# Kernel optimization log

Hardware: AMD Instinct MI355X
Metric: run time of the kernel (lower is better)

## Reference

```python
import jax, jax.numpy as jnp
import numpy as np

B, T, D, V, L = 32, 512, 512, 1024, 128
BLANK = 0
NEG = -1e30  # log-domain 'minus infinity' that is fp-safe


def setup_inputs() -> dict:
    key = jax.random.key(0)
    k1, k2, k3 = jax.random.split(key, 3)
    x = jax.random.normal(k1, (B, T, D), dtype=jnp.float32)
    W = jax.random.normal(k2, (D, V), dtype=jnp.float32) / np.sqrt(D).astype(np.float32)
    b = jnp.zeros((V,), dtype=jnp.float32)
    # CTC targets must be in [1, V) (never the blank id 0)
    target = jax.random.randint(k3, (B, L), 1, V)
    input_lengths = jnp.full((B,), T, dtype=jnp.int32)
    target_lengths = jnp.full((B,), L, dtype=jnp.int32)
    return {"x": x, "W": W, "b": b, "target": target,
            "input_lengths": input_lengths, "target_lengths": target_lengths}


def _ctc_loss(log_probs, target, input_lengths, target_lengths):
    # log_probs: [T, B, V] (time-major), target: [B, L]
    Tt, Bb, _ = log_probs.shape
    Ll = target.shape[1]
    S = 2 * Ll + 1  # extended label sequence: blank,t0,blank,t1,...,blank
    ext = jnp.full((Bb, S), BLANK, dtype=target.dtype).at[:, 1::2].set(target)  # [B,S]
    ext_m2 = jnp.pad(ext, ((0, 0), (2, 0)), constant_values=BLANK)[:, :S]
    skip = (ext != BLANK) & (ext != ext_m2) & (jnp.arange(S)[None, :] >= 2)  # [B,S]

    # gather log-probs of extended labels for every time step: [T,B,S]
    lp_ext = jnp.take_along_axis(log_probs, jnp.broadcast_to(ext[None], (Tt, Bb, S)), axis=2)

    alpha0 = jnp.full((Bb, S), NEG, log_probs.dtype)
    alpha0 = alpha0.at[:, 0].set(lp_ext[0, :, 0]).at[:, 1].set(lp_ext[0, :, 1])

    def step(alpha, lp_t):
        a1 = jnp.pad(alpha, ((0, 0), (1, 0)), constant_values=NEG)[:, :S]
        a2 = jnp.pad(alpha, ((0, 0), (2, 0)), constant_values=NEG)[:, :S]
        c = jnp.logaddexp(alpha, a1)
        c = jnp.where(skip, jnp.logaddexp(c, a2), c)
        new = c + lp_t
        return new, new

    _, alphas = jax.lax.scan(step, alpha0, lp_ext[1:])
    alphas = jnp.concatenate([alpha0[None], alphas], axis=0)  # [T,B,S]

    bi = jnp.arange(Bb)
    a_last = alphas[input_lengths - 1, bi]  # [B,S] alpha at each sample's final frame
    ll = jnp.logaddexp(a_last[bi, 2 * target_lengths - 1], a_last[bi, 2 * target_lengths])
    nll = -ll  # per-sample negative log-likelihood
    # zero_infinity=True: infinite losses are zeroed
    nll = jnp.where(jnp.isinf(nll) | (nll > 1e29), 0.0, nll)
    # reduction='mean': divide each loss by its target length, then mean
    return jnp.mean(nll / jnp.maximum(target_lengths, 1).astype(nll.dtype))


def reference(x, W, b, target, input_lengths, target_lengths):
    logits = jnp.einsum('btd,dv->btv', x, W) + b  # nn.Linear
    log_probs = jax.nn.log_softmax(logits, axis=-1)  # [B,T,V]
    return _ctc_loss(jnp.transpose(log_probs, (1, 0, 2)), target, input_lengths, target_lengths)
```

## Files before the change

kernel.cpp:

```cpp
#include <hip/hip_runtime.h>
#include <cstdint>


#define SPAD 260
#define PEXT_PAD_ROWS 64
#define L2E 1.4426950408889634f
#define LN2 0.6931471805599453f

typedef short v8s __attribute__((ext_vector_type(8)));
typedef float v4f __attribute__((ext_vector_type(4)));

__device__ __forceinline__ uint32_t f2bf_bits(float f) {
  uint32_t u = __float_as_uint(f);
  return (u + 0x7FFFu + ((u >> 16) & 1u)) >> 16;
}
__device__ __forceinline__ float bf2f(uint32_t h) { return __uint_as_float(h << 16); }

__global__ void k_prep(const float* __restrict__ x, uint16_t* __restrict__ xb, long long n,
                       const float* __restrict__ W, uint16_t* __restrict__ Wt, int D, int V,
                       float* __restrict__ out, int nconv) {
  if (blockIdx.x == 0 && threadIdx.x == 0) out[0] = 0.f;
  if ((int)blockIdx.x < nconv) {
    long long i = ((long long)blockIdx.x * blockDim.x + threadIdx.x) * 8;
    if (i >= n) return;
    float4 a = *(const float4*)(x + i);
    float4 b = *(const float4*)(x + i + 4);
    uint4 o;
    o.x = f2bf_bits(a.x) | (f2bf_bits(a.y) << 16);
    o.y = f2bf_bits(a.z) | (f2bf_bits(a.w) << 16);
    o.z = f2bf_bits(b.x) | (f2bf_bits(b.y) << 16);
    o.w = f2bf_bits(b.z) | (f2bf_bits(b.w) << 16);
    *(uint4*)(xb + i) = o;
  } else {
    __shared__ float tile[32][33];
    const int bid2 = blockIdx.x - nconv;
    const int n0 = (bid2 % (V / 32)) * 32, k0 = (bid2 / (V / 32)) * 32;
    const int tx = threadIdx.x & 31, ty = threadIdx.x >> 5;
    #pragma unroll
    for (int i = 0; i < 32; i += 8)
      tile[ty + i][tx] = W[(size_t)(k0 + ty + i) * V + n0 + tx];
    __syncthreads();
    #pragma unroll
    for (int i = 0; i < 32; i += 8)
      Wt[(size_t)(n0 + ty + i) * D + k0 + tx] = (uint16_t)f2bf_bits(tile[tx][ty + i]);
  }
}

__global__ __launch_bounds__(256) void k_gemm(const uint16_t* __restrict__ A,
                                              const uint16_t* __restrict__ Bt,
                                              const float* __restrict__ bias,
                                              uint16_t* __restrict__ C, int M, int N, int K) {
  __shared__ uint16_t As[128 * 32];
  __shared__ uint16_t Bs[128 * 32];
  const int tid = threadIdx.x, lane = tid & 63, wave = tid >> 6;
  const int m0 = blockIdx.x * 128, n0 = blockIdx.y * 128;
  const int wm = wave & 1, wn = wave >> 1;
  const int frow = lane & 15, kb = lane >> 4;
  const int lr = lane >> 2, kc = lane & 3;
  v4f acc[4][4] = {};

  for (int k0 = 0; k0 < K; k0 += 32) {
    __syncthreads();
    #pragma unroll
    for (int i = 0; i < 2; i++) {
      const int r = (wave * 2 + i) * 16 + lr;
      const uint16_t* ga = A + (size_t)(m0 + r) * K + k0 + kc * 8;
      const uint16_t* gb = Bt + (size_t)(n0 + r) * K + k0 + kc * 8;
      __builtin_amdgcn_global_load_lds(
          (const __attribute__((address_space(1))) void*)ga,
          (__attribute__((address_space(3))) void*)(As + (wave * 2 + i) * 512 + lane * 8), 16, 0, 0);
      __builtin_amdgcn_global_load_lds(
          (const __attribute__((address_space(1))) void*)gb,
          (__attribute__((address_space(3))) void*)(Bs + (wave * 2 + i) * 512 + lane * 8), 16, 0, 0);
    }
    __syncthreads();

    v8s af[4], bf[4];
    #pragma unroll
    for (int i = 0; i < 4; i++)
      af[i] = *(const v8s*)(As + (wm * 64 + i * 16 + frow) * 32 + kb * 8);
    #pragma unroll
    for (int j = 0; j < 4; j++)
      bf[j] = *(const v8s*)(Bs + (wn * 64 + j * 16 + frow) * 32 + kb * 8);
    #pragma unroll
    for (int i = 0; i < 4; i++)
      #pragma unroll
      for (int j = 0; j < 4; j++)
        acc[i][j] = __builtin_amdgcn_mfma_f32_16x16x32_bf16(af[i], bf[j], acc[i][j], 0, 0, 0);
  }

  const int crow = (lane >> 4) * 4, ccol = lane & 15;
  #pragma unroll
  for (int j = 0; j < 4; j++) {
    const int n = n0 + wn * 64 + j * 16 + ccol;
    const float bv = bias[n];
    #pragma unroll
    for (int i = 0; i < 4; i++) {
      const int mb = m0 + wm * 64 + i * 16 + crow;
      #pragma unroll
      for (int r2 = 0; r2 < 4; r2++)
        C[(size_t)(mb + r2) * N + n] = (uint16_t)f2bf_bits(acc[i][j][r2] + bv);
    }
  }
}

__global__ void k_softmax_gather(const uint16_t* __restrict__ logits, const int* __restrict__ target,
                                 const int* __restrict__ tlen, float* __restrict__ pext,
                                 int T, int V, int L) {
  const int row = blockIdx.x * 4 + (threadIdx.x >> 6);
  const int lane = threadIdx.x & 63;
  const uint16_t* lrow = logits + (size_t)row * V;

  float xs[16];
  int cnt = 0;
  float mx = -INFINITY;
  for (int base = 0; base < V; base += 256) {
    const int idx = base + lane * 4;
    uint2 u = *(const uint2*)(lrow + idx);
    float4 v;
    v.x = bf2f(u.x & 0xFFFFu); v.y = bf2f(u.x >> 16);
    v.z = bf2f(u.y & 0xFFFFu); v.w = bf2f(u.y >> 16);
    xs[cnt] = v.x; xs[cnt + 1] = v.y; xs[cnt + 2] = v.z; xs[cnt + 3] = v.w; cnt += 4;
    mx = fmaxf(mx, fmaxf(fmaxf(v.x, v.y), fmaxf(v.z, v.w)));
  }
  #pragma unroll
  for (int off = 32; off; off >>= 1) mx = fmaxf(mx, __shfl_xor(mx, off, 64));
  float sum = 0.f;
  #pragma unroll
  for (int q = 0; q < 16; q++) { if (q < cnt) sum += exp2f((xs[q] - mx) * L2E); }
  #pragma unroll
  for (int off = 32; off; off >>= 1) sum += __shfl_xor(sum, off, 64);
  const float lse2 = mx * L2E + log2f(sum);

  const int bidx = row / T;
  const int Lb = tlen[bidx];
  const int S = 2 * Lb + 1;
  float* prow = pext + (size_t)row * SPAD;
  for (int s = lane; s < SPAD; s += 64) {
    float p = 0.f;
    if (s < S) {
      const int lbl = (s & 1) ? target[bidx * L + ((s - 1) >> 1)] : 0;
      p = exp2f(bf2f(lrow[lbl]) * L2E - lse2);
    }
    prow[s] = p;
  }
}

__device__ __forceinline__ float wave_shr1(float x) {
  return __int_as_float(__builtin_amdgcn_update_dpp(0, __float_as_int(x), 0x138, 0xf, 0xf, true));
}
__device__ __forceinline__ float wave_max_nonneg(float x) {
  x = fmaxf(x, __int_as_float(__builtin_amdgcn_update_dpp(0, __float_as_int(x), 0x111, 0xf, 0xf, true)));
  x = fmaxf(x, __int_as_float(__builtin_amdgcn_update_dpp(0, __float_as_int(x), 0x112, 0xf, 0xf, true)));
  x = fmaxf(x, __int_as_float(__builtin_amdgcn_update_dpp(0, __float_as_int(x), 0x114, 0xf, 0xf, true)));
  x = fmaxf(x, __int_as_float(__builtin_amdgcn_update_dpp(0, __float_as_int(x), 0x118, 0xf, 0xf, true)));
  x = fmaxf(x, __int_as_float(__builtin_amdgcn_update_dpp(0, __float_as_int(x), 0x142, 0xf, 0xf, true)));
  x = fmaxf(x, __int_as_float(__builtin_amdgcn_update_dpp(0, __float_as_int(x), 0x143, 0xf, 0xf, true)));
  return __int_as_float(__builtin_amdgcn_readlane(__float_as_int(x), 63));
}

__device__ __forceinline__ void load8(float4* __restrict__ p, float* __restrict__ p4,
                                      const float* __restrict__ pb, int t0, int lane) {
  #pragma unroll
  for (int k = 0; k < 8; k++) {
    const float* row = pb + (size_t)(t0 + k) * SPAD;
    p[k] = *(const float4*)(row + (lane << 2));
    p4[k] = row[256];
  }
}

__global__ __launch_bounds__(64, 1) void k_ctc(const float* __restrict__ pext,
                                               const int* __restrict__ target,
                                               const int* __restrict__ ilen,
                                               const int* __restrict__ tlen,
                                               float* __restrict__ out, int T, int L) {
  const int b = blockIdx.x;
  const int lane = threadIdx.x;
  const int B = gridDim.x;
  const int Tb = ilen[b];
  const int Lb = tlen[b];
  const int S = 2 * Lb + 1;
  const int* tg = target + b * L;

  const int s1 = 4 * lane + 1, s3 = 4 * lane + 3;
  float sk1 = 0.f, sk3 = 0.f;
  if (s1 >= 3 && s1 < S) sk1 = (tg[(s1 - 1) >> 1] != tg[(s1 - 3) >> 1]) ? 1.f : 0.f;
  if (s3 >= 3 && s3 < S) sk3 = (tg[(s3 - 1) >> 1] != tg[(s3 - 3) >> 1]) ? 1.f : 0.f;

  const float* pb = pext + (size_t)b * T * SPAD;
  const float4 p0 = *(const float4*)(pb + (lane << 2));
  float a0 = (lane == 0) ? p0.x : 0.f;
  float a1 = (lane == 0) ? p0.y : 0.f;
  float a2 = 0.f, a3 = 0.f, a4 = 0.f;
  float log2C = 0.f;

  #define CTC_STEP(PP, P4) {                                            \
    const float pm3 = wave_shr1(a3);                                    \
    const float a255 = __int_as_float(__builtin_amdgcn_readlane(__float_as_int(a3), 63)); \
    const float n0v = (a0 + pm3) * (PP).x;                              \
    const float n1v = (a1 + a0 + sk1 * pm3) * (PP).y;                   \
    const float n2v = (a2 + a1) * (PP).z;                               \
    const float n3v = (a3 + a2 + sk3 * a1) * (PP).w;                    \
    const float n4v = (a4 + a255) * (P4);                               \
    a0 = n0v; a1 = n1v; a2 = n2v; a3 = n3v; a4 = n4v; }

  #define RENORM {                                                      \
    float m = fmaxf(fmaxf(fmaxf(a0, a1), fmaxf(a2, a3)), a4);           \
    m = wave_max_nonneg(m);                                             \
    const int e = (int)((__float_as_uint(m) >> 23) & 255u) - 127;       \
    const float scale = __uint_as_float((uint32_t)(127 - e) << 23);     \
    a0 *= scale; a1 *= scale; a2 *= scale; a3 *= scale; a4 *= scale;    \
    log2C += (float)e; }

  float4 Pa[8], Pb_[8], Pc[8], Pd[8];
  float Qa[8], Qb[8], Qc[8], Qd[8];
  int t0 = 1;
  bool done = false;
  load8(Pa, Qa, pb, t0, lane);
  load8(Pb_, Qb, pb, t0 + 8, lane);
  load8(Pc, Qc, pb, t0 + 16, lane);

  #define PHASE(LP, LQ, CP, CQ) {                                       \
    if (t0 + 8 <= Tb) {                                                 \
      load8(LP, LQ, pb, t0 + 24, lane);                                 \
      _Pragma("unroll")                                                 \
      for (int k = 0; k < 8; k++) CTC_STEP(CP[k], CQ[k]);               \
      RENORM; t0 += 8;                                                  \
    } else {                                                            \
      _Pragma("unroll")                                                 \
      for (int k = 0; k < 8; k++) { if (t0 + k < Tb) CTC_STEP(CP[k], CQ[k]); } \
      RENORM; done = true;                                              \
    } }

  while (!done) {
    PHASE(Pd, Qd, Pa, Qa); if (done) break;
    PHASE(Pa, Qa, Pb_, Qb); if (done) break;
    PHASE(Pb_, Qb, Pc, Qc); if (done) break;
    PHASE(Pc, Qc, Pd, Qd);
  }

  __shared__ float abuf[257];
  abuf[4 * lane + 0] = a0; abuf[4 * lane + 1] = a1;
  abuf[4 * lane + 2] = a2; abuf[4 * lane + 3] = a3;
  if (lane == 63) abuf[256] = a4;
  __syncthreads();
  if (lane == 0) {
    const float ssum = abuf[2 * Lb - 1] + abuf[2 * Lb];
    const float ll = (log2f(ssum) + log2C) * LN2;
    float nll = -ll;
    if (!(nll < 1e29f)) nll = 0.f;
    atomicAdd(out, nll / ((float)(Lb > 0 ? Lb : 1) * (float)B));
  }
}

extern "C" void kernel_launch(void* const* d_in, const int* in_sizes, int n_in,
                              void* d_out, int out_size, void* d_ws, size_t ws_size,
                              hipStream_t stream) {
  const float* x      = (const float*)d_in[0];
  const float* W      = (const float*)d_in[1];
  const float* bias   = (const float*)d_in[2];
  const int*  target  = (const int*)d_in[3];
  const int*  ilen    = (const int*)d_in[4];
  const int*  tlen    = (const int*)d_in[5];

  const int B = in_sizes[4];
  const int V = in_sizes[2];
  const int D = in_sizes[1] / V;
  const int T = in_sizes[0] / (B * D);
  const int L = in_sizes[3] / B;
  const int M = B * T;

  char* ws = (char*)d_ws;
  const size_t xb_bytes = (size_t)M * D * 2;
  const size_t wt_bytes = (size_t)V * D * 2;
  const size_t pext_bytes = (size_t)(M + PEXT_PAD_ROWS) * SPAD * 4;
  uint16_t* xb = (uint16_t*)ws;
  uint16_t* Wt = (uint16_t*)(ws + xb_bytes);
  uint16_t* logits = (uint16_t*)(ws + xb_bytes + wt_bytes);
  const size_t log_bytes = (size_t)M * V * 2;

  float* pext;
  if (pext_bytes <= xb_bytes + wt_bytes) {
    pext = (float*)ws;
  } else {
    pext = (float*)(ws + xb_bytes + wt_bytes + log_bytes);
  }

  const long long nx = (long long)M * D;
  const int nconv = (int)((nx / 8 + 255) / 256);
  const int ntrans = (V / 32) * (D / 32);
  k_prep<<<nconv + ntrans, 256, 0, stream>>>(x, xb, nx, W, Wt, D, V, (float*)d_out, nconv);
  k_gemm<<<dim3(M / 128, V / 128), 256, 0, stream>>>(xb, Wt, bias, logits, M, V, D);
  k_softmax_gather<<<M / 4, 256, 0, stream>>>(logits, target, tlen, pext, T, V, L);
  k_ctc<<<B, 64, 0, stream>>>(pext, target, ilen, tlen, (float*)d_out, T, L);
}
```

Baseline: 169.9 us.

## Fuse x conversion, GEMM, log-softmax and label gather into one kernel

Replaces the separate x-to-bf16 conversion, tiled GEMM and softmax/gather kernels with one kernel in which each block computes a full 32-row by 1024-column logits tile. The block converts x on the fly, takes the row max and sum-exp from registers, and gathers the label probabilities from an LDS tile. This removes the round trips of the bf16 x copy and the full logits matrix through global memory, plus two launches. In exchange it drops LDS staging of operands, so W fragments are read straight from global/L2 with little reuse. It also uses a large LDS tile and 128 accumulator registers per thread, which limits occupancy to about one block per CU.

```diff
diff --git a/kernel.cpp b/kernel.cpp
--- a/kernel.cpp
+++ b/kernel.cpp
@@ -4,6 +4,7 @@
 
 #define SPAD 260
 #define PEXT_PAD_ROWS 64
+#define TSTRIDE 36
 #define L2E 1.4426950408889634f
 #define LN2 0.6931471805599453f
 
@@ -16,133 +17,134 @@
 }
 __device__ __forceinline__ float bf2f(uint32_t h) { return __uint_as_float(h << 16); }
 
-__global__ void k_prep(const float* __restrict__ x, uint16_t* __restrict__ xb, long long n,
-                       const float* __restrict__ W, uint16_t* __restrict__ Wt, int D, int V,
-                       float* __restrict__ out, int nconv) {
+__device__ __forceinline__ v8s pack_bf8(float4 lo, float4 hi) {
+  union { v8s v; uint16_t s[8]; } u;
+  u.s[0] = (uint16_t)f2bf_bits(lo.x); u.s[1] = (uint16_t)f2bf_bits(lo.y);
+  u.s[2] = (uint16_t)f2bf_bits(lo.z); u.s[3] = (uint16_t)f2bf_bits(lo.w);
+  u.s[4] = (uint16_t)f2bf_bits(hi.x); u.s[5] = (uint16_t)f2bf_bits(hi.y);
+  u.s[6] = (uint16_t)f2bf_bits(hi.z); u.s[7] = (uint16_t)f2bf_bits(hi.w);
+  return u.v;
+}
+
+__global__ void k_prep(const float* __restrict__ W, uint16_t* __restrict__ Wt, int D, int V,
+                       float* __restrict__ out) {
   if (blockIdx.x == 0 && threadIdx.x == 0) out[0] = 0.f;
-  if ((int)blockIdx.x < nconv) {
-    long long i = ((long long)blockIdx.x * blockDim.x + threadIdx.x) * 8;
-    if (i >= n) return;
-    float4 a = *(const float4*)(x + i);
-    float4 b = *(const float4*)(x + i + 4);
-    uint4 o;
-    o.x = f2bf_bits(a.x) | (f2bf_bits(a.y) << 16);
-    o.y = f2bf_bits(a.z) | (f2bf_bits(a.w) << 16);
-    o.z = f2bf_bits(b.x) | (f2bf_bits(b.y) << 16);
-    o.w = f2bf_bits(b.z) | (f2bf_bits(b.w) << 16);
-    *(uint4*)(xb + i) = o;
-  } else {
-    __shared__ float tile[32][33];
-    const int bid2 = blockIdx.x - nconv;
-    const int n0 = (bid2 % (V / 32)) * 32, k0 = (bid2 / (V / 32)) * 32;
-    const int tx = threadIdx.x & 31, ty = threadIdx.x >> 5;
-    #pragma unroll
-    for (int i = 0; i < 32; i += 8)
-      tile[ty + i][tx] = W[(size_t)(k0 + ty + i) * V + n0 + tx];
-    __syncthreads();
-    #pragma unroll
-    for (int i = 0; i < 32; i += 8)
-      Wt[(size_t)(n0 + ty + i) * D + k0 + tx] = (uint16_t)f2bf_bits(tile[tx][ty + i]);
-  }
-}
-
-__global__ __launch_bounds__(256) void k_gemm(const uint16_t* __restrict__ A,
-                                              const uint16_t* __restrict__ Bt,
-                                              const float* __restrict__ bias,
-                                              uint16_t* __restrict__ C, int M, int N, int K) {
-  __shared__ uint16_t As[128 * 32];
-  __shared__ uint16_t Bs[128 * 32];
+  __shared__ float tile[32][33];
+  const int n0 = (blockIdx.x % (V / 32)) * 32, k0 = (blockIdx.x / (V / 32)) * 32;
+  const int tx = threadIdx.x & 31, ty = threadIdx.x >> 5;
+  #pragma unroll
+  for (int i = 0; i < 32; i += 8)
+    tile[ty + i][tx] = W[(size_t)(k0 + ty + i) * V + n0 + tx];
+  __syncthreads();
+  #pragma unroll
+  for (int i = 0; i < 32; i += 8)
+    Wt[(size_t)(n0 + ty + i) * D + k0 + tx] = (uint16_t)f2bf_bits(tile[tx][ty + i]);
+}
+
+__global__ __launch_bounds__(256, 1) void k_fused(const float* __restrict__ x,
+                                                  const uint16_t* __restrict__ Wt,
+                                                  const float* __restrict__ bias,
+                                                  const int* __restrict__ target,
+                                                  const int* __restrict__ tlen,
+                                                  float* __restrict__ pext,
+                                                  int T, int V, int K, int L) {
   const int tid = threadIdx.x, lane = tid & 63, wave = tid >> 6;
-  const int m0 = blockIdx.x * 128, n0 = blockIdx.y * 128;
-  const int wm = wave & 1, wn = wave >> 1;
-  const int frow = lane & 15, kb = lane >> 4;
-  const int lr = lane >> 2, kc = lane & 3;
-  v4f acc[4][4] = {};
+  const int q = lane >> 4, c = lane & 15;
+  const int m0 = blockIdx.x * 32;
+  const int nw = wave * 256;
+
+  v4f acc[2][16] = {};
+
+  const float* xa0 = x + (size_t)(m0 + c) * K + q * 8;
+  const float* xa1 = x + (size_t)(m0 + 16 + c) * K + q * 8;
 
   for (int k0 = 0; k0 < K; k0 += 32) {
-    __syncthreads();
-    #pragma unroll
-    for (int i = 0; i < 2; i++) {
-      const int r = (wave * 2 + i) * 16 + lr;
-      const uint16_t* ga = A + (size_t)(m0 + r) * K + k0 + kc * 8;
-      const uint16_t* gb = Bt + (size_t)(n0 + r) * K + k0 + kc * 8;
-      __builtin_amdgcn_global_load_lds(
-          (const __attribute__((address_space(1))) void*)ga,
-          (__attribute__((address_space(3))) void*)(As + (wave * 2 + i) * 512 + lane * 8), 16, 0, 0);
-      __builtin_amdgcn_global_load_lds(
-          (const __attribute__((address_space(1))) void*)gb,
-          (__attribute__((address_space(3))) void*)(Bs + (wave * 2 + i) * 512 + lane * 8), 16, 0, 0);
-    }
-    __syncthreads();
-
-    v8s af[4], bf[4];
-    #pragma unroll
-    for (int i = 0; i < 4; i++)
-      af[i] = *(const v8s*)(As + (wm * 64 + i * 16 + frow) * 32 + kb * 8);
-    #pragma unroll
-    for (int j = 0; j < 4; j++)
-      bf[j] = *(const v8s*)(Bs + (wn * 64 + j * 16 + frow) * 32 + kb * 8);
-    #pragma unroll
-    for (int i = 0; i < 4; i++)
-      #pragma unroll
-      for (int j = 0; j < 4; j++)
-        acc[i][j] = __builtin_amdgcn_mfma_f32_16x16x32_bf16(af[i], bf[j], acc[i][j], 0, 0, 0);
-  }
-
-  const int crow = (lane >> 4) * 4, ccol = lane & 15;
-  #pragma unroll
-  for (int j = 0; j < 4; j++) {
-    const int n = n0 + wn * 64 + j * 16 + ccol;
-    const float bv = bias[n];
-    #pragma unroll
-    for (int i = 0; i < 4; i++) {
-      const int mb = m0 + wm * 64 + i * 16 + crow;
-      #pragma unroll
-      for (int r2 = 0; r2 < 4; r2++)
-        C[(size_t)(mb + r2) * N + n] = (uint16_t)f2bf_bits(acc[i][j][r2] + bv);
-    }
-  }
-}
-
-__global__ void k_softmax_gather(const uint16_t* __restrict__ logits, const int* __restrict__ target,
-                                 const int* __restrict__ tlen, float* __restrict__ pext,
-                                 int T, int V, int L) {
-  const int row = blockIdx.x * 4 + (threadIdx.x >> 6);
-  const int lane = threadIdx.x & 63;
-  const uint16_t* lrow = logits + (size_t)row * V;
-
-  float xs[16];
-  int cnt = 0;
-  float mx = -INFINITY;
-  for (int base = 0; base < V; base += 256) {
-    const int idx = base + lane * 4;
-    uint2 u = *(const uint2*)(lrow + idx);
-    float4 v;
-    v.x = bf2f(u.x & 0xFFFFu); v.y = bf2f(u.x >> 16);
-    v.z = bf2f(u.y & 0xFFFFu); v.w = bf2f(u.y >> 16);
-    xs[cnt] = v.x; xs[cnt + 1] = v.y; xs[cnt + 2] = v.z; xs[cnt + 3] = v.w; cnt += 4;
-    mx = fmaxf(mx, fmaxf(fmaxf(v.x, v.y), fmaxf(v.z, v.w)));
-  }
-  #pragma unroll
-  for (int off = 32; off; off >>= 1) mx = fmaxf(mx, __shfl_xor(mx, off, 64));
-  float sum = 0.f;
-  #pragma unroll
-  for (int q = 0; q < 16; q++) { if (q < cnt) sum += exp2f((xs[q] - mx) * L2E); }
-  #pragma unroll
-  for (int off = 32; off; off >>= 1) sum += __shfl_xor(sum, off, 64);
-  const float lse2 = mx * L2E + log2f(sum);
-
-  const int bidx = row / T;
-  const int Lb = tlen[bidx];
+    const v8s af0 = pack_bf8(*(const float4*)(xa0 + k0), *(const float4*)(xa0 + k0 + 4));
+    const v8s af1 = pack_bf8(*(const float4*)(xa1 + k0), *(const float4*)(xa1 + k0 + 4));
+    #pragma unroll
+    for (int jj = 0; jj < 16; jj++) {
+      const v8s bf = *(const v8s*)(Wt + (size_t)(nw + jj * 16 + c) * K + k0 + q * 8);
+      acc[0][jj] = __builtin_amdgcn_mfma_f32_16x16x32_bf16(af0, bf, acc[0][jj], 0, 0, 0);
+      acc[1][jj] = __builtin_amdgcn_mfma_f32_16x16x32_bf16(af1, bf, acc[1][jj], 0, 0, 0);
+    }
+  }
+
+  float bv[16];
+  #pragma unroll
+  for (int jj = 0; jj < 16; jj++) bv[jj] = bias[nw + jj * 16 + c];
+  #pragma unroll
+  for (int i = 0; i < 2; i++)
+    #pragma unroll
+    for (int jj = 0; jj < 16; jj++)
+      #pragma unroll
+      for (int r = 0; r < 4; r++) acc[i][jj][r] += bv[jj];
+
+  float mx[2][4], sm[2][4];
+  #pragma unroll
+  for (int i = 0; i < 2; i++)
+    #pragma unroll
+    for (int r = 0; r < 4; r++) {
+      float m = -INFINITY;
+      #pragma unroll
+      for (int jj = 0; jj < 16; jj++) m = fmaxf(m, acc[i][jj][r]);
+      #pragma unroll
+      for (int off = 1; off < 16; off <<= 1) m = fmaxf(m, __shfl_xor(m, off, 64));
+      float s = 0.f;
+      #pragma unroll
+      for (int jj = 0; jj < 16; jj++) s += exp2f((acc[i][jj][r] - m) * L2E);
+      #pragma unroll
+      for (int off = 1; off < 16; off <<= 1) s += __shfl_xor(s, off, 64);
+      mx[i][r] = m; sm[i][r] = s;
+    }
+
+  __shared__ uint16_t ltile[1024 * TSTRIDE];
+  __shared__ float red_mx[4][32], red_sm[4][32], lse2s[32];
+
+  #pragma unroll
+  for (int i = 0; i < 2; i++)
+    #pragma unroll
+    for (int jj = 0; jj < 16; jj++) {
+      union { uint16_t s[4]; uint64_t u; } pk;
+      #pragma unroll
+      for (int r = 0; r < 4; r++) pk.s[r] = (uint16_t)f2bf_bits(acc[i][jj][r]);
+      *(uint64_t*)(ltile + (size_t)(nw + jj * 16 + c) * TSTRIDE + i * 16 + 4 * q) = pk.u;
+    }
+  if (c == 0) {
+    #pragma unroll
+    for (int i = 0; i < 2; i++)
+      #pragma unroll
+      for (int r = 0; r < 4; r++) {
+        red_mx[wave][16 * i + 4 * q + r] = mx[i][r];
+        red_sm[wave][16 * i + 4 * q + r] = sm[i][r];
+      }
+  }
+  __syncthreads();
+  if (tid < 32) {
+    float M = fmaxf(fmaxf(red_mx[0][tid], red_mx[1][tid]), fmaxf(red_mx[2][tid], red_mx[3][tid]));
+    float S = 0.f;
+    #pragma unroll
+    for (int w = 0; w < 4; w++) S += red_sm[w][tid] * exp2f((red_mx[w][tid] - M) * L2E);
+    lse2s[tid] = M * L2E + log2f(S);
+  }
+  __syncthreads();
+
+  const int b = m0 / T;
+  const int Lb = tlen[b];
   const int S = 2 * Lb + 1;
-  float* prow = pext + (size_t)row * SPAD;
-  for (int s = lane; s < SPAD; s += 64) {
-    float p = 0.f;
-    if (s < S) {
-      const int lbl = (s & 1) ? target[bidx * L + ((s - 1) >> 1)] : 0;
-      p = exp2f(bf2f(lrow[lbl]) * L2E - lse2);
-    }
-    prow[s] = p;
+  const int* tg = target + b * L;
+  #pragma unroll
+  for (int rr = 0; rr < 8; rr++) {
+    const int row = wave * 8 + rr;
+    const float l2 = lse2s[row];
+    float* prow = pext + (size_t)(m0 + row) * SPAD;
+    for (int s = lane; s < SPAD; s += 64) {
+      float p = 0.f;
+      if (s < S) {
+        const int lbl = (s & 1) ? tg[(s - 1) >> 1] : 0;
+        p = exp2f(bf2f(ltile[(size_t)lbl * TSTRIDE + row]) * L2E - l2);
+      }
+      prow[s] = p;
+    }
   }
 }
 
@@ -271,26 +273,11 @@
   const int M = B * T;
 
   char* ws = (char*)d_ws;
-  const size_t xb_bytes = (size_t)M * D * 2;
   const size_t wt_bytes = (size_t)V * D * 2;
-  const size_t pext_bytes = (size_t)(M + PEXT_PAD_ROWS) * SPAD * 4;
-  uint16_t* xb = (uint16_t*)ws;
-  uint16_t* Wt = (uint16_t*)(ws + xb_bytes);
-  uint16_t* logits = (uint16_t*)(ws + xb_bytes + wt_bytes);
-  const size_t log_bytes = (size_t)M * V * 2;
-
-  float* pext;
-  if (pext_bytes <= xb_bytes + wt_bytes) {
-    pext = (float*)ws;
-  } else {
-    pext = (float*)(ws + xb_bytes + wt_bytes + log_bytes);
-  }
-
-  const long long nx = (long long)M * D;
-  const int nconv = (int)((nx / 8 + 255) / 256);
-  const int ntrans = (V / 32) * (D / 32);
-  k_prep<<<nconv + ntrans, 256, 0, stream>>>(x, xb, nx, W, Wt, D, V, (float*)d_out, nconv);
-  k_gemm<<<dim3(M / 128, V / 128), 256, 0, stream>>>(xb, Wt, bias, logits, M, V, D);
-  k_softmax_gather<<<M / 4, 256, 0, stream>>>(logits, target, tlen, pext, T, V, L);
+  uint16_t* Wt = (uint16_t*)ws;
+  float* pext = (float*)(ws + wt_bytes);
+
+  k_prep<<<(V / 32) * (D / 32), 256, 0, stream>>>(W, Wt, D, V, (float*)d_out);
+  k_fused<<<M / 32, 256, 0, stream>>>(x, Wt, bias, target, tlen, pext, T, V, D, L);
   k_ctc<<<B, 64, 0, stream>>>(pext, target, ilen, tlen, (float*)d_out, T, L);
 }
```

After: 279.6 us. 1.65x slower.

## Restructure GEMM to stage full-K A tile in LDS and stream B from global

Applied to the files above, without the earlier changes.

The GEMM now uses a 64x256 block tile. The full 64xK A slab is loaded into padded LDS once, and each wave reads its B fragments straight from global memory. This removes the per-K-step double syncthreads and the shared B staging. The trade-off is a larger LDS footprint, which limits occupancy, and uncoalesced global B fragment loads. Separately, scheduling barriers are added in the CTC recurrence so the prefetch loads are issued before the compute steps.

```diff
diff --git a/kernel.cpp b/kernel.cpp
--- a/kernel.cpp
+++ b/kernel.cpp
@@ -4,6 +4,7 @@
 
 #define SPAD 260
 #define PEXT_PAD_ROWS 64
+#define ASTR 520
 #define L2E 1.4426950408889634f
 #define LN2 0.6931471805599453f
 
@@ -50,53 +51,47 @@
                                               const uint16_t* __restrict__ Bt,
                                               const float* __restrict__ bias,
                                               uint16_t* __restrict__ C, int M, int N, int K) {
-  __shared__ uint16_t As[128 * 32];
-  __shared__ uint16_t Bs[128 * 32];
+  __shared__ uint16_t As[64 * ASTR];
   const int tid = threadIdx.x, lane = tid & 63, wave = tid >> 6;
-  const int m0 = blockIdx.x * 128, n0 = blockIdx.y * 128;
-  const int wm = wave & 1, wn = wave >> 1;
+  const int m0 = blockIdx.x * 64, n0 = blockIdx.y * 256;
   const int frow = lane & 15, kb = lane >> 4;
-  const int lr = lane >> 2, kc = lane & 3;
   v4f acc[4][4] = {};
 
+  #pragma unroll
+  for (int i = 0; i < 16; i++) {
+    const int r = i * 4 + wave;
+    const uint16_t* ga = A + (size_t)(m0 + r) * K + lane * 8;
+    __builtin_amdgcn_global_load_lds(
+        (const __attribute__((address_space(1))) void*)ga,
+        (__attribute__((address_space(3))) void*)(As + r * ASTR + lane * 8), 16, 0, 0);
+  }
+  __syncthreads();
+
+  const uint16_t* Bw = Bt + (size_t)(n0 + wave * 64) * K;
+  #pragma unroll 2
   for (int k0 = 0; k0 < K; k0 += 32) {
-    __syncthreads();
-    #pragma unroll
-    for (int i = 0; i < 2; i++) {
-      const int r = (wave * 2 + i) * 16 + lr;
-      const uint16_t* ga = A + (size_t)(m0 + r) * K + k0 + kc * 8;
-      const uint16_t* gb = Bt + (size_t)(n0 + r) * K + k0 + kc * 8;
-      __builtin_amdgcn_global_load_lds(
-          (const __attribute__((address_space(1))) void*)ga,
-          (__attribute__((address_space(3))) void*)(As + (wave * 2 + i) * 512 + lane * 8), 16, 0, 0);
-      __builtin_amdgcn_global_load_lds(
-          (const __attribute__((address_space(1))) void*)gb,
-          (__attribute__((address_space(3))) void*)(Bs + (wave * 2 + i) * 512 + lane * 8), 16, 0, 0);
-    }
-    __syncthreads();
-
-    v8s af[4], bf[4];
+    v8s bfr[4], af[4];
+    #pragma unroll
+    for (int j = 0; j < 4; j++)
+      bfr[j] = *(const v8s*)(Bw + (size_t)(j * 16 + frow) * K + k0 + kb * 8);
     #pragma unroll
     for (int i = 0; i < 4; i++)
-      af[i] = *(const v8s*)(As + (wm * 64 + i * 16 + frow) * 32 + kb * 8);
-    #pragma unroll
-    for (int j = 0; j < 4; j++)
-      bf[j] = *(const v8s*)(Bs + (wn * 64 + j * 16 + frow) * 32 + kb * 8);
+      af[i] = *(const v8s*)(As + (i * 16 + frow) * ASTR + k0 + kb * 8);
     #pragma unroll
     for (int i = 0; i < 4; i++)
       #pragma unroll
       for (int j = 0; j < 4; j++)
-        acc[i][j] = __builtin_amdgcn_mfma_f32_16x16x32_bf16(af[i], bf[j], acc[i][j], 0, 0, 0);
+        acc[i][j] = __builtin_amdgcn_mfma_f32_16x16x32_bf16(af[i], bfr[j], acc[i][j], 0, 0, 0);
   }
 
   const int crow = (lane >> 4) * 4, ccol = lane & 15;
   #pragma unroll
   for (int j = 0; j < 4; j++) {
-    const int n = n0 + wn * 64 + j * 16 + ccol;
+    const int n = n0 + wave * 64 + j * 16 + ccol;
     const float bv = bias[n];
     #pragma unroll
     for (int i = 0; i < 4; i++) {
-      const int mb = m0 + wm * 64 + i * 16 + crow;
+      const int mb = m0 + i * 16 + crow;
       #pragma unroll
       for (int r2 = 0; r2 < 4; r2++)
         C[(size_t)(mb + r2) * N + n] = (uint16_t)f2bf_bits(acc[i][j][r2] + bv);
@@ -219,10 +214,12 @@
   load8(Pa, Qa, pb, t0, lane);
   load8(Pb_, Qb, pb, t0 + 8, lane);
   load8(Pc, Qc, pb, t0 + 16, lane);
+  __builtin_amdgcn_sched_barrier(0);
 
   #define PHASE(LP, LQ, CP, CQ) {                                       \
     if (t0 + 8 <= Tb) {                                                 \
       load8(LP, LQ, pb, t0 + 24, lane);                                 \
+      __builtin_amdgcn_sched_barrier(0);                                \
       _Pragma("unroll")                                                 \
       for (int k = 0; k < 8; k++) CTC_STEP(CP[k], CQ[k]);               \
       RENORM; t0 += 8;                                                  \
@@ -290,7 +287,7 @@
   const int nconv = (int)((nx / 8 + 255) / 256);
   const int ntrans = (V / 32) * (D / 32);
   k_prep<<<nconv + ntrans, 256, 0, stream>>>(x, xb, nx, W, Wt, D, V, (float*)d_out, nconv);
-  k_gemm<<<dim3(M / 128, V / 128), 256, 0, stream>>>(xb, Wt, bias, logits, M, V, D);
+  k_gemm<<<dim3(M / 64, V / 256), 256, 0, stream>>>(xb, Wt, bias, logits, M, V, D);
   k_softmax_gather<<<M / 4, 256, 0, stream>>>(logits, target, tlen, pext, T, V, L);
   k_ctc<<<B, 64, 0, stream>>>(pext, target, ilen, tlen, (float*)d_out, T, L);
 }
```

Result: slower. 182.6 us (+7.5%).
